# Kernel optimization log

Measured on AMD Instinct MI355X. Metric: run time of the kernel, lower is better.

The kernel has to match this reference:

```python
import jax, jax.numpy as jnp
import numpy as np

L, B, T, D, H, FF = 4, 8, 1024, 256, 8, 1024
DK = D // H
SCALE = 1.0 / np.sqrt(DK)


def _ln(x, g, b, eps=1e-6):
    m = jnp.mean(x, axis=-1, keepdims=True)
    v = jnp.mean(jnp.square(x - m), axis=-1, keepdims=True)
    return (x - m) * jax.lax.rsqrt(v + eps) * g + b


def _l2norm(x, eps=1e-8):
    n = jnp.sqrt(jnp.sum(jnp.square(x), axis=-1, keepdims=True))
    return x / jnp.maximum(n, eps)


def setup_inputs() -> dict:
    key = jax.random.key(0)
    ks = jax.random.split(key, 8)
    s = 0.02
    inp = {
        'x': jax.random.normal(ks[0], (B, T, D), dtype=jnp.float32),
        'padding_mask': jnp.zeros((B, T), dtype=bool),
        'ln1_g': jnp.ones((L, D), jnp.float32), 'ln1_b': jnp.zeros((L, D), jnp.float32),
        'qn_g': jnp.ones((L, D), jnp.float32), 'qn_b': jnp.zeros((L, D), jnp.float32),
        'Wqkv': jax.random.normal(ks[1], (L, 3 * D, D), jnp.float32) * s,
        'bqkv': jnp.zeros((L, 3 * D), jnp.float32),
        'Wo': jax.random.normal(ks[2], (L, D, D), jnp.float32) * s,
        'bo': jnp.zeros((L, D), jnp.float32),
        'ln2_g': jnp.ones((L, D), jnp.float32), 'ln2_b': jnp.zeros((L, D), jnp.float32),
        'W1': jax.random.normal(ks[3], (L, FF, D), jnp.float32) * s,
        'b1': jnp.zeros((L, FF), jnp.float32),
        'W2': jax.random.normal(ks[4], (L, D, FF), jnp.float32) * s,
        'b2': jnp.zeros((L, D), jnp.float32),
        'alpha': jnp.full((L,), 0.1, jnp.float32),
        'beta': jnp.full((L,), 0.1, jnp.float32),
    }
    return inp


def _block(x, pad_mask, p):
    (g1, bb1, qg, qb, wqkv, bqkv, wo, bo, g2, bb2, w1, b1, w2, b2, a, be) = p
    Bn, Tn, Dn = x.shape
    # --- SemiCausalAttention on norm1(x) ---
    xn = _ln(x, g1, bb1)
    h = _ln(xn, qg, qb)                      # q_norm LayerNorm
    qkv = h @ wqkv.T + bqkv                  # [B,T,3D]
    qkv = qkv.reshape(Bn, Tn, 3, H, DK).transpose(2, 0, 3, 1, 4)  # [3,B,H,T,dk]
    Q, K, V = qkv[0], qkv[1], qkv[2]
    Q = _l2norm(Q)
    K = _l2norm(K)
    scores = jnp.einsum('bhtd,bhsd->bhts', Q, K) * SCALE
    scores = jnp.clip(scores, -10.0, 10.0)
    causal = jnp.triu(jnp.ones((Tn, Tn), dtype=bool), k=1)        # True = future
    scores = jnp.where(causal[None, None], -10000.0, scores)
    scores = jnp.where(pad_mask[:, None, None, :], -10000.0, scores)
    attn = jax.nn.softmax(scores, axis=-1)
    ao = jnp.einsum('bhts,bhsd->bhtd', attn, V)                   # [B,H,T,dk]
    ao = ao.transpose(0, 2, 1, 3).reshape(Bn, Tn, Dn)
    attn_out = (ao @ wo.T + bo) * 0.5
    x = x + jnp.tanh(a) * attn_out
    # --- FFN ---
    f = _ln(x, g2, bb2)
    f = jax.nn.gelu(f @ w1.T + b1, approximate=False)
    f = f @ w2.T + b2
    x = x + jnp.tanh(be) * f
    return jnp.clip(x, -100.0, 100.0)


def reference(x, padding_mask, ln1_g, ln1_b, qn_g, qn_b, Wqkv, bqkv, Wo, bo,
              ln2_g, ln2_b, W1, b1, W2, b2, alpha, beta):
    params = (ln1_g, ln1_b, qn_g, qn_b, Wqkv, bqkv, Wo, bo,
              ln2_g, ln2_b, W1, b1, W2, b2, alpha, beta)

    def step(carry, p):
        return _block(carry, padding_mask, p), None

    out, _ = jax.lax.scan(step, x, params)
    return out
```

## Files before the change

kernel.cpp:

```cpp
#include <hip/hip_runtime.h>
#include <hip/hip_bf16.h>
#include <math.h>

#define BB 8
#define TT 1024
#define DD 256
#define HH 8
#define BT 8192

typedef __attribute__((ext_vector_type(4))) float f32x4;
typedef __attribute__((ext_vector_type(16))) float f32x16;
typedef __attribute__((ext_vector_type(8))) short short8;
typedef __attribute__((ext_vector_type(4))) short short4v;
typedef __attribute__((ext_vector_type(8))) __bf16 bf16x8;

__device__ inline float bf2f(short s) {
  unsigned int u = ((unsigned int)(unsigned short)s) << 16;
  return __builtin_bit_cast(float, u);
}
__device__ inline short f2bf(float f) {
  unsigned int u = __builtin_bit_cast(unsigned int, f);
  unsigned int lsb = (u >> 16) & 1u;
  u += 0x7fffu + lsb;
  return (short)(u >> 16);
}
__device__ inline unsigned int cvtpk(float lo, float hi) {
  unsigned int r;
  asm("v_cvt_pk_bf16_f32 %0, %1, %2" : "=v"(r) : "v"(lo), "v"(hi));
  return r;
}

__device__ inline f32x4 mfma16(short8 a, short8 b, f32x4 c) {
  return __builtin_amdgcn_mfma_f32_16x16x32_bf16(
      __builtin_bit_cast(bf16x8, a), __builtin_bit_cast(bf16x8, b), c, 0, 0, 0);
}
__device__ inline f32x16 mfma32(short8 a, short8 b, f32x16 c) {
  return __builtin_amdgcn_mfma_f32_32x32x16_bf16(
      __builtin_bit_cast(bf16x8, a), __builtin_bit_cast(bf16x8, b), c, 0, 0, 0);
}

__device__ inline void gload_lds16(void* lds, const void* g) {
  __builtin_amdgcn_global_load_lds(
      (const __attribute__((address_space(1))) unsigned int*)g,
      (__attribute__((address_space(3))) unsigned int*)lds, 16, 0, 0);
}

__global__ __launch_bounds__(256) void cvt_all(
    const float4* __restrict__ s0, short4v* __restrict__ d0, int n0,
    const float4* __restrict__ s1, short4v* __restrict__ d1, int n1,
    const float4* __restrict__ s2, short4v* __restrict__ d2, int n2,
    const float4* __restrict__ s3, short4v* __restrict__ d3, int n3)
{
  int i = blockIdx.x * 256 + threadIdx.x;
  const float4* s; short4v* d;
  if (i < n0) { s = s0 + i; d = d0 + i; }
  else if ((i -= n0) < n1) { s = s1 + i; d = d1 + i; }
  else if ((i -= n1) < n2) { s = s2 + i; d = d2 + i; }
  else if ((i -= n2) < n3) { s = s3 + i; d = d3 + i; }
  else return;
  float4 v = *s;
  short4v o;
  o[0] = f2bf(v.x); o[1] = f2bf(v.y); o[2] = f2bf(v.z); o[3] = f2bf(v.w);
  *d = o;
}

__global__ __launch_bounds__(256) void ln_kernel(
    const float* __restrict__ Xin,
    const float* __restrict__ g1, const float* __restrict__ b1,
    const float* __restrict__ g2, const float* __restrict__ b2,
    short* __restrict__ out)
{
  const int row = blockIdx.x * 4 + (threadIdx.x >> 6);
  const int lane = threadIdx.x & 63;
  const float4 v = *(const float4*)(Xin + (size_t)row * 256 + lane * 4);
  float y[4] = {v.x, v.y, v.z, v.w};

  float s = y[0] + y[1] + y[2] + y[3];
  #pragma unroll
  for (int m = 32; m >= 1; m >>= 1) s += __shfl_xor(s, m, 64);
  float mean = s * (1.0f / 256.0f);
  float sq = 0.f;
  #pragma unroll
  for (int i = 0; i < 4; ++i) { y[i] -= mean; sq += y[i] * y[i]; }
  #pragma unroll
  for (int m = 32; m >= 1; m >>= 1) sq += __shfl_xor(sq, m, 64);
  float rs = rsqrtf(sq * (1.0f / 256.0f) + 1e-6f);
  #pragma unroll
  for (int i = 0; i < 4; ++i) y[i] = y[i] * rs * g1[lane * 4 + i] + b1[lane * 4 + i];

  float s2 = y[0] + y[1] + y[2] + y[3];
  #pragma unroll
  for (int m = 32; m >= 1; m >>= 1) s2 += __shfl_xor(s2, m, 64);
  float m2 = s2 * (1.0f / 256.0f);
  float sq2 = 0.f;
  #pragma unroll
  for (int i = 0; i < 4; ++i) { y[i] -= m2; sq2 += y[i] * y[i]; }
  #pragma unroll
  for (int m = 32; m >= 1; m >>= 1) sq2 += __shfl_xor(sq2, m, 64);
  float rs2 = rsqrtf(sq2 * (1.0f / 256.0f) + 1e-6f);
  #pragma unroll
  for (int i = 0; i < 4; ++i) y[i] = y[i] * rs2 * g2[lane * 4 + i] + b2[lane * 4 + i];

  #pragma unroll
  for (int i = 0; i < 4; ++i) out[(size_t)row * 256 + lane * 4 + i] = f2bf(y[i]);
}

__global__ __launch_bounds__(256) void vtr_kernel(
    const short* __restrict__ qkv, short* __restrict__ vT)
{
  __shared__ short T_s[32][264];
  const int tid = threadIdx.x;
  const int bh = blockIdx.x >> 2;
  const int tc = blockIdx.x & 3;
  const int b = bh >> 3, h = bh & 7;
  const int t = tc * 256 + tid;
  const short* src = qkv + ((size_t)b * TT + t) * 768 + 512 + h * 32;
  short8 v0 = *(const short8*)(src);
  short8 v1 = *(const short8*)(src + 8);
  short8 v2 = *(const short8*)(src + 16);
  short8 v3 = *(const short8*)(src + 24);
  #pragma unroll
  for (int d = 0; d < 8; ++d) {
    T_s[d][tid] = v0[d];
    T_s[d + 8][tid] = v1[d];
    T_s[d + 16][tid] = v2[d];
    T_s[d + 24][tid] = v3[d];
  }
  __syncthreads();
  const int d = tid >> 3, toff = (tid & 7) * 32;
  short* dst = vT + ((size_t)bh * 32 + d) * 1024 + tc * 256 + toff;
  #pragma unroll
  for (int s = 0; s < 4; ++s)
    *(short8*)(dst + s * 8) = *(const short8*)&T_s[d][toff + s * 8];
}

template<int BN, int EPI>
__global__ __launch_bounds__(256) void gemm_bt(
    const short* __restrict__ A, const short* __restrict__ Bw,
    const float* __restrict__ bias, float* __restrict__ X,
    short* __restrict__ Obf, const float* __restrict__ scale_p,
    int M, int N, int K)
{
  constexpr int MI = (BN == 128) ? 4 : 2;
  __shared__ __align__(16) short A_s[128 * 128];
  __shared__ __align__(16) short B_s[BN * 128];
  const int tid = threadIdx.x;
  const int lane = tid & 63;
  const int w = tid >> 6;
  const int lo4 = lane & 15, hi2 = lane >> 4;
  int wm, wn0;
  if (BN == 128) { wm = (w >> 1) * 64; wn0 = (w & 1) * 64; }
  else           { wm = w * 32;        wn0 = 0; }
  const int bid = blockIdx.x + blockIdx.y * gridDim.x;
  const int nwg = gridDim.x * gridDim.y;
  const int wg = (bid & 7) * (nwg >> 3) + (bid >> 3);
  const int tM = (wg / gridDim.x) * 128, tN = (wg % gridDim.x) * BN;

  f32x4 acc[MI][4];
  #pragma unroll
  for (int i = 0; i < MI; ++i)
    #pragma unroll
    for (int j = 0; j < 4; ++j) acc[i][j] = (f32x4){0.f, 0.f, 0.f, 0.f};

  const int rswzA = ((wm + lo4) & 7) << 3;
  for (int k0 = 0; k0 < K; k0 += 128) {
    #pragma unroll
    for (int ri = 0; ri < 8; ++ri) {
      int o = ri * 2048 + tid * 8;
      int row = o >> 7;
      int col = (o & 127) ^ ((row & 7) << 3);
      gload_lds16(&A_s[ri * 2048 + w * 512], A + (size_t)(tM + row) * K + k0 + col);
    }
    #pragma unroll
    for (int ri = 0; ri < BN / 16; ++ri) {
      int o = ri * 2048 + tid * 8;
      int row = o >> 7;
      int col = (o & 127) ^ ((row & 7) << 3);
      gload_lds16(&B_s[ri * 2048 + w * 512], Bw + (size_t)(tN + row) * K + k0 + col);
    }
    __syncthreads();
    #pragma unroll
    for (int kc = 0; kc < 4; ++kc) {
      short8 af[MI], bfr[4];
      #pragma unroll
      for (int i = 0; i < MI; ++i) {
        int row = wm + i * 16 + lo4;
        af[i] = *(const short8*)&A_s[row * 128 + ((kc * 32 + hi2 * 8) ^ ((row & 7) << 3))];
      }
      #pragma unroll
      for (int j = 0; j < 4; ++j) {
        int row = wn0 + j * 16 + lo4;
        bfr[j] = *(const short8*)&B_s[row * 128 + ((kc * 32 + hi2 * 8) ^ ((row & 7) << 3))];
      }
      #pragma unroll
      for (int i = 0; i < MI; ++i)
        #pragma unroll
        for (int j = 0; j < 4; ++j)
          acc[i][j] = mfma16(af[i], bfr[j], acc[i][j]);
    }
    __syncthreads();
  }
  (void)rswzA;

  if (EPI == 4) {
    #pragma unroll
    for (int i = 0; i < MI; ++i)
      #pragma unroll
      for (int j = 0; j < 4; ++j)
        #pragma unroll
        for (int r = 0; r < 4; ++r)
          acc[i][j][r] += bias[tN + wn0 + j * 16 + lo4];
    if (tN < 512) {
      const float C2 = 0.25503489702966368f;
      const float sc = (tN < 256) ? C2 : 1.0f;
      #pragma unroll
      for (int i = 0; i < MI; ++i) {
        #pragma unroll
        for (int r = 0; r < 4; ++r) {
          float s01 = acc[i][0][r] * acc[i][0][r] + acc[i][1][r] * acc[i][1][r];
          float s23 = acc[i][2][r] * acc[i][2][r] + acc[i][3][r] * acc[i][3][r];
          #pragma unroll
          for (int m = 1; m <= 8; m <<= 1) {
            s01 += __shfl_xor(s01, m, 64);
            s23 += __shfl_xor(s23, m, 64);
          }
          float n01 = sc / fmaxf(sqrtf(s01), 1e-8f);
          float n23 = sc / fmaxf(sqrtf(s23), 1e-8f);
          acc[i][0][r] *= n01; acc[i][1][r] *= n01;
          acc[i][2][r] *= n23; acc[i][3][r] *= n23;
        }
      }
    }
    #pragma unroll
    for (int i = 0; i < MI; ++i)
      #pragma unroll
      for (int j = 0; j < 4; ++j)
        #pragma unroll
        for (int r = 0; r < 4; ++r) {
          int row = tM + wm + i * 16 + hi2 * 4 + r;
          int col = tN + wn0 + j * 16 + lo4;
          Obf[(size_t)row * N + col] = f2bf(acc[i][j][r]);
        }
    return;
  }

  #pragma unroll
  for (int i = 0; i < MI; ++i) {
    #pragma unroll
    for (int j = 0; j < 4; ++j) {
      #pragma unroll
      for (int r = 0; r < 4; ++r) {
        int row = tM + wm + i * 16 + hi2 * 4 + r;
        int col = tN + wn0 + j * 16 + lo4;
        float v = acc[i][j][r] + bias[col];
        size_t idx = (size_t)row * N + col;
        if (EPI == 2) {
          float gl = 0.5f * v * (1.0f + erff(v * 0.70710678118f));
          Obf[idx] = f2bf(gl);
        } else {
          Obf[idx] = f2bf(v);
        }
      }
    }
  }
}

template<int MODE>
__global__ __launch_bounds__(256) void gemm_ln(
    const short* __restrict__ A, const short* __restrict__ Bw,
    const float* __restrict__ bias, float* __restrict__ X,
    short* __restrict__ Obf, const float* __restrict__ scale_p,
    const float* __restrict__ gA, const float* __restrict__ bA,
    const float* __restrict__ gB, const float* __restrict__ bB,
    int K, int doLN)
{
  __shared__ __align__(16) short A_s[32 * 128];
  __shared__ __align__(16) short B_s[256 * 128];
  __shared__ float Red[2][32][4][2];
  const int tid = threadIdx.x;
  const int lane = tid & 63;
  const int w = tid >> 6;
  const int lo4 = lane & 15, hi2 = lane >> 4;
  const int tM = blockIdx.x * 32;

  f32x4 acc[2][4];
  #pragma unroll
  for (int i = 0; i < 2; ++i)
    #pragma unroll
    for (int j = 0; j < 4; ++j) acc[i][j] = (f32x4){0.f, 0.f, 0.f, 0.f};

  for (int k0 = 0; k0 < K; k0 += 128) {
    #pragma unroll
    for (int ri = 0; ri < 2; ++ri) {
      int o = ri * 2048 + tid * 8;
      int row = o >> 7;
      int col = (o & 127) ^ ((row & 7) << 3);
      gload_lds16(&A_s[ri * 2048 + w * 512], A + (size_t)(tM + row) * K + k0 + col);
    }
    #pragma unroll
    for (int ri = 0; ri < 16; ++ri) {
      int o = ri * 2048 + tid * 8;
      int row = o >> 7;
      int col = (o & 127) ^ ((row & 7) << 3);
      gload_lds16(&B_s[ri * 2048 + w * 512], Bw + (size_t)row * K + k0 + col);
    }
    __syncthreads();
    #pragma unroll
    for (int kc = 0; kc < 4; ++kc) {
      short8 af[2], bfr[4];
      #pragma unroll
      for (int i = 0; i < 2; ++i) {
        int row = i * 16 + lo4;
        af[i] = *(const short8*)&A_s[row * 128 + ((kc * 32 + hi2 * 8) ^ ((row & 7) << 3))];
      }
      #pragma unroll
      for (int j = 0; j < 4; ++j) {
        int row = w * 64 + j * 16 + lo4;
        bfr[j] = *(const short8*)&B_s[row * 128 + ((kc * 32 + hi2 * 8) ^ ((row & 7) << 3))];
      }
      #pragma unroll
      for (int i = 0; i < 2; ++i)
        #pragma unroll
        for (int j = 0; j < 4; ++j)
          acc[i][j] = mfma16(af[i], bfr[j], acc[i][j]);
    }
    __syncthreads();
  }

  const float ts = tanhf(scale_p[0]);
  float xv[2][4][4];
  #pragma unroll
  for (int i = 0; i < 2; ++i)
    #pragma unroll
    for (int j = 0; j < 4; ++j)
      #pragma unroll
      for (int r = 0; r < 4; ++r) {
        int row = i * 16 + hi2 * 4 + r;
        int col = w * 64 + j * 16 + lo4;
        float v = acc[i][j][r] + bias[col];
        size_t idx = (size_t)(tM + row) * 256 + col;
        float xn;
        if (MODE == 0) {
          xn = X[idx] + ts * 0.5f * v;
        } else {
          xn = X[idx] + ts * v;
          xn = fminf(100.f, fmaxf(-100.f, xn));
        }
        X[idx] = xn;
        xv[i][j][r] = xn;
      }

  if (!doLN) return;

  #pragma unroll
  for (int i = 0; i < 2; ++i)
    #pragma unroll
    for (int r = 0; r < 4; ++r) {
      float s = xv[i][0][r] + xv[i][1][r] + xv[i][2][r] + xv[i][3][r];
      float q = xv[i][0][r] * xv[i][0][r] + xv[i][1][r] * xv[i][1][r]
              + xv[i][2][r] * xv[i][2][r] + xv[i][3][r] * xv[i][3][r];
      #pragma unroll
      for (int m = 1; m <= 8; m <<= 1) { s += __shfl_xor(s, m, 64); q += __shfl_xor(q, m, 64); }
      if (lo4 == 0) { Red[0][i * 16 + hi2 * 4 + r][w][0] = s; Red[0][i * 16 + hi2 * 4 + r][w][1] = q; }
    }
  __syncthreads();
  #pragma unroll
  for (int i = 0; i < 2; ++i)
    #pragma unroll
    for (int r = 0; r < 4; ++r) {
      int row = i * 16 + hi2 * 4 + r;
      float s = Red[0][row][0][0] + Red[0][row][1][0] + Red[0][row][2][0] + Red[0][row][3][0];
      float q = Red[0][row][0][1] + Red[0][row][1][1] + Red[0][row][2][1] + Red[0][row][3][1];
      float mu = s * (1.0f / 256.0f);
      float var = q * (1.0f / 256.0f) - mu * mu;
      float rs = rsqrtf(var + 1e-6f);
      #pragma unroll
      for (int j = 0; j < 4; ++j) {
        int col = w * 64 + j * 16 + lo4;
        xv[i][j][r] = (xv[i][j][r] - mu) * rs * gA[col] + bA[col];
      }
    }

  if (MODE == 1) {
    #pragma unroll
    for (int i = 0; i < 2; ++i)
      #pragma unroll
      for (int r = 0; r < 4; ++r) {
        float s = xv[i][0][r] + xv[i][1][r] + xv[i][2][r] + xv[i][3][r];
        float q = xv[i][0][r] * xv[i][0][r] + xv[i][1][r] * xv[i][1][r]
                + xv[i][2][r] * xv[i][2][r] + xv[i][3][r] * xv[i][3][r];
        #pragma unroll
        for (int m = 1; m <= 8; m <<= 1) { s += __shfl_xor(s, m, 64); q += __shfl_xor(q, m, 64); }
        if (lo4 == 0) { Red[1][i * 16 + hi2 * 4 + r][w][0] = s; Red[1][i * 16 + hi2 * 4 + r][w][1] = q; }
      }
    __syncthreads();
    #pragma unroll
    for (int i = 0; i < 2; ++i)
      #pragma unroll
      for (int r = 0; r < 4; ++r) {
        int row = i * 16 + hi2 * 4 + r;
        float s = Red[1][row][0][0] + Red[1][row][1][0] + Red[1][row][2][0] + Red[1][row][3][0];
        float q = Red[1][row][0][1] + Red[1][row][1][1] + Red[1][row][2][1] + Red[1][row][3][1];
        float mu = s * (1.0f / 256.0f);
        float var = q * (1.0f / 256.0f) - mu * mu;
        float rs = rsqrtf(var + 1e-6f);
        #pragma unroll
        for (int j = 0; j < 4; ++j) {
          int col = w * 64 + j * 16 + lo4;
          xv[i][j][r] = (xv[i][j][r] - mu) * rs * gB[col] + bB[col];
        }
      }
  }

  #pragma unroll
  for (int i = 0; i < 2; ++i)
    #pragma unroll
    for (int j = 0; j < 4; ++j)
      #pragma unroll
      for (int r = 0; r < 4; ++r) {
        int row = i * 16 + hi2 * 4 + r;
        int col = w * 64 + j * 16 + lo4;
        Obf[(size_t)(tM + row) * 256 + col] = f2bf(xv[i][j][r]);
      }
}

__device__ __forceinline__ void pv_acc(const unsigned int* PKO, int half_,
                                       short8 vb, int hi1, f32x16& acc) {
  unsigned int keep0 = hi1 ? PKO[4 * half_ + 2] : PKO[4 * half_ + 0];
  unsigned int keep1 = hi1 ? PKO[4 * half_ + 3] : PKO[4 * half_ + 1];
  unsigned int send0 = hi1 ? PKO[4 * half_ + 0] : PKO[4 * half_ + 2];
  unsigned int send1 = hi1 ? PKO[4 * half_ + 1] : PKO[4 * half_ + 3];
  unsigned int r0 = (unsigned int)__shfl_xor((int)send0, 32, 64);
  unsigned int r1 = (unsigned int)__shfl_xor((int)send1, 32, 64);
  union { unsigned int u[4]; short8 s; } fa;
  fa.u[0] = hi1 ? r0 : keep0;
  fa.u[1] = hi1 ? r1 : keep1;
  fa.u[2] = hi1 ? keep0 : r0;
  fa.u[3] = hi1 ? keep1 : r1;
  acc = mfma32(fa.s, vb, acc);
}

template<bool KG1, bool M0, bool M1>
__device__ __forceinline__ void attn_tile(
    int t, const short* __restrict__ Kbase, const short* __restrict__ VTl,
    const short8* qb, unsigned int pm0, unsigned int pm1, int lo5, int hi1,
    f32x16& oaccA, f32x16& oaccB, float& rsum)
{
  const short* kp0 = Kbase + (size_t)(t * 64 + lo5) * 768;
  short8 k00 = *(const short8*)(kp0 + hi1 * 8);
  short8 k01 = *(const short8*)(kp0 + 16 + hi1 * 8);
  short8 k10, k11;
  if (KG1) {
    const short* kp1 = Kbase + (size_t)(t * 64 + 32 + lo5) * 768;
    k10 = *(const short8*)(kp1 + hi1 * 8);
    k11 = *(const short8*)(kp1 + 16 + hi1 * 8);
  }
  const short* vp = VTl + t * 64 + hi1 * 8;
  short8 vb0 = *(const short8*)(vp);
  short8 vb1 = *(const short8*)(vp + 16);
  short8 vb2, vb3;
  if (KG1) {
    vb2 = *(const short8*)(vp + 32);
    vb3 = *(const short8*)(vp + 48);
  }
  unsigned int pk0[8], pk1[8];
  {
    f32x16 z = (f32x16)0.0f;
    z = mfma32(k00, qb[0], z);
    z = mfma32(k01, qb[1], z);
    float pr[16];
    #pragma unroll
    for (int r = 0; r < 16; ++r) {
      float sv = __builtin_amdgcn_fmed3f(z[r], -14.4269504f, 14.4269504f);
      float pe;
      asm("v_exp_f32 %0, %1" : "=v"(pe) : "v"(sv));
      const int keyrel = (r & 3) + 8 * (r >> 2) + 4 * hi1;
      if (M0) pe = (keyrel > lo5) ? 0.f : pe;
      if (pm0) pe = ((pm0 >> keyrel) & 1u) ? 0.f : pe;
      pr[r] = pe;
      rsum += pe;
    }
    #pragma unroll
    for (int i = 0; i < 8; ++i) pk0[i] = cvtpk(pr[2 * i], pr[2 * i + 1]);
  }
  if (KG1) {
    f32x16 z = (f32x16)0.0f;
    z = mfma32(k10, qb[0], z);
    z = mfma32(k11, qb[1], z);
    float pr[16];
    #pragma unroll
    for (int r = 0; r < 16; ++r) {
      float sv = __builtin_amdgcn_fmed3f(z[r], -14.4269504f, 14.4269504f);
      float pe;
      asm("v_exp_f32 %0, %1" : "=v"(pe) : "v"(sv));
      const int keyrel = (r & 3) + 8 * (r >> 2) + 4 * hi1;
      if (M1) pe = (keyrel > lo5) ? 0.f : pe;
      if (pm1) pe = ((pm1 >> keyrel) & 1u) ? 0.f : pe;
      pr[r] = pe;
      rsum += pe;
    }
    #pragma unroll
    for (int i = 0; i < 8; ++i) pk1[i] = cvtpk(pr[2 * i], pr[2 * i + 1]);
  }
  pv_acc(pk0, 0, vb0, hi1, oaccA);
  pv_acc(pk0, 1, vb1, hi1, oaccB);
  if (KG1) {
    pv_acc(pk1, 0, vb2, hi1, oaccA);
    pv_acc(pk1, 1, vb3, hi1, oaccB);
  }
}

__global__ __launch_bounds__(256, 2) void attn_kernel(
    const short* __restrict__ qkv, const short* __restrict__ vT,
    const unsigned char* __restrict__ pad, short* __restrict__ ao)
{
  __shared__ float Red[2][17][64];
  const int tid = threadIdx.x, lane = tid & 63, w = tid >> 6;
  const int lo5 = lane & 31, hi1 = lane >> 5;
  const int bid = blockIdx.x;
  const int b = bid & 7;
  const int h = (bid >> 3) & 7;
  const int bj = bid >> 6;
  const int p = w >> 1;
  const int half = w & 1;
  const int j = p ? (31 - bj) : bj;
  const size_t rowbase = (size_t)b * TT;
  const int qrow = j * 32 + lo5;
  const int ntile = (j >> 1) + 1;

  const short* Kbase = qkv + rowbase * 768 + 256 + h * 32;
  const short* VTl = vT + ((size_t)(b * 8 + h) * 32 + lo5) * 1024;

  const ulonglong2 pv = *(const ulonglong2*)(pad + rowbase + lane * 16);
  const unsigned long long anyp = __ballot((pv.x | pv.y) != 0ull);

  short8 qb[2];
  #pragma unroll
  for (int c2 = 0; c2 < 2; ++c2)
    qb[c2] = *(const short8*)(qkv + (rowbase + qrow) * 768 + h * 32 + c2 * 16 + hi1 * 8);

  f32x16 oaccA = (f32x16)0.0f;
  f32x16 oaccB = (f32x16)0.0f;
  float rsum = 0.f;

  for (int t = half; t < ntile; t += 2) {
    unsigned long long pm = 0;
    if ((anyp >> (4 * t)) & 0xFull)
      pm = __ballot(pad[rowbase + t * 64 + lane] != 0);
    unsigned int pm0 = (unsigned int)pm, pm1 = (unsigned int)(pm >> 32);
    if (t + 1 < ntile)
      attn_tile<true, false, false>(t, Kbase, VTl, qb, pm0, pm1, lo5, hi1, oaccA, oaccB, rsum);
    else if (j & 1)
      attn_tile<true, false, true>(t, Kbase, VTl, qb, pm0, pm1, lo5, hi1, oaccA, oaccB, rsum);
    else
      attn_tile<false, true, false>(t, Kbase, VTl, qb, pm0, pm1, lo5, hi1, oaccA, oaccB, rsum);
  }

  if (half) {
    #pragma unroll
    for (int r = 0; r < 16; ++r) Red[p][r][lane] = oaccA[r] + oaccB[r];
    Red[p][16][lane] = rsum;
  }
  __syncthreads();
  if (!half) {
    #pragma unroll
    for (int r = 0; r < 16; ++r) oaccA[r] += oaccB[r] + Red[p][r][lane];
    rsum += Red[p][16][lane];
    rsum += __shfl_xor(rsum, 32, 64);
    float rinv = 1.0f / fmaxf(rsum, 1e-30f);
    #pragma unroll
    for (int r = 0; r < 16; ++r) {
      int ql = (r & 3) + 8 * (r >> 2) + 4 * hi1;
      float riv = __shfl(rinv, ql, 64);
      int qg = j * 32 + ql;
      ao[(rowbase + qg) * 256 + h * 32 + lo5] = f2bf(oaccA[r] * riv);
    }
  }
}

extern "C" void kernel_launch(void* const* d_in, const int* in_sizes, int n_in,
                              void* d_out, int out_size, void* d_ws, size_t ws_size,
                              hipStream_t stream) {
  const float* x_in  = (const float*)d_in[0];
  const unsigned char* pad = (const unsigned char*)d_in[1];
  const float* ln1_g = (const float*)d_in[2];
  const float* ln1_b = (const float*)d_in[3];
  const float* qn_g  = (const float*)d_in[4];
  const float* qn_b  = (const float*)d_in[5];
  const float* Wqkv  = (const float*)d_in[6];
  const float* bqkv  = (const float*)d_in[7];
  const float* Wo    = (const float*)d_in[8];
  const float* bo    = (const float*)d_in[9];
  const float* ln2_g = (const float*)d_in[10];
  const float* ln2_b = (const float*)d_in[11];
  const float* W1    = (const float*)d_in[12];
  const float* b1    = (const float*)d_in[13];
  const float* W2    = (const float*)d_in[14];
  const float* b2    = (const float*)d_in[15];
  const float* alpha = (const float*)d_in[16];
  const float* beta  = (const float*)d_in[17];

  char* ws = (char*)d_ws;
  size_t off = 0;
  short* wqkv_bf = (short*)(ws + off); off += (size_t)4 * 768 * 256 * 2;
  short* wo_bf   = (short*)(ws + off); off += (size_t)4 * 256 * 256 * 2;
  short* w1_bf   = (short*)(ws + off); off += (size_t)4 * 1024 * 256 * 2;
  short* w2_bf   = (short*)(ws + off); off += (size_t)4 * 256 * 1024 * 2;
  short* h_bf    = (short*)(ws + off); off += (size_t)BT * 256 * 2;
  short* qkv_bf  = (short*)(ws + off); off += (size_t)BT * 768 * 2;
  short* ao_bf   = (short*)(ws + off); off += (size_t)BT * 256 * 2;
  short* g_bf    = (short*)(ws + off); off += (size_t)BT * 1024 * 2;
  short* vT_bf   = (short*)(ws + off); off += (size_t)BT * 256 * 2;

  float* X = (float*)d_out;

  hipMemcpyAsync(d_out, x_in, (size_t)BT * DD * 4, hipMemcpyDeviceToDevice, stream);
  cvt_all<<<3072, 256, 0, stream>>>(
      (const float4*)Wqkv, (short4v*)wqkv_bf, 4 * 768 * 256 / 4,
      (const float4*)Wo,   (short4v*)wo_bf,   4 * 256 * 256 / 4,
      (const float4*)W1,   (short4v*)w1_bf,   4 * 1024 * 256 / 4,
      (const float4*)W2,   (short4v*)w2_bf,   4 * 256 * 1024 / 4);

  ln_kernel<<<2048, 256, 0, stream>>>(X, ln1_g, ln1_b, qn_g, qn_b, h_bf);

  for (int l = 0; l < 4; ++l) {
    gemm_bt<128, 4><<<dim3(6, 64), 256, 0, stream>>>(h_bf, wqkv_bf + (size_t)l * 768 * 256,
                                                     bqkv + l * 768, nullptr, qkv_bf, nullptr,
                                                     8192, 768, 256);
    vtr_kernel<<<256, 256, 0, stream>>>(qkv_bf, vT_bf);
    attn_kernel<<<1024, 256, 0, stream>>>(qkv_bf, vT_bf, pad, ao_bf);
    gemm_ln<0><<<256, 256, 0, stream>>>(ao_bf, wo_bf + (size_t)l * 256 * 256,
                                        bo + l * 256, X, h_bf, alpha + l,
                                        ln2_g + l * 256, ln2_b + l * 256,
                                        nullptr, nullptr, 256, 1);
    gemm_bt<128, 2><<<dim3(8, 64), 256, 0, stream>>>(h_bf, w1_bf + (size_t)l * 1024 * 256,
                                                     b1 + l * 1024, nullptr, g_bf, nullptr,
                                                     8192, 1024, 256);
    const int nl = (l < 3) ? (l + 1) : 0;
    gemm_ln<1><<<256, 256, 0, stream>>>(g_bf, w2_bf + (size_t)l * 256 * 1024,
                                        b2 + l * 256, X, h_bf, beta + l,
                                        ln1_g + nl * 256, ln1_b + nl * 256,
                                        qn_g + nl * 256, qn_b + nl * 256,
                                        1024, (l < 3) ? 1 : 0);
  }
}
```

Before: 380.7 us.

## Write Q/K/V head-major from QKV GEMM and double-buffer GEMM K-tiles

The QKV GEMM epilogue now scatters Q, K and V into separate head-major [B*H, T, 32] buffers, so attention and the V transpose read contiguous 64-byte rows instead of 768-element strided rows. Separately, both GEMM kernels switch from a single 128-wide K tile to double-buffered 64-wide K tiles, issuing the next tile's loads before computing the current one to overlap memory with MFMA. LDS footprint stays the same. The epilogue stores become more scattered, and the loop has twice as many barriers.

```diff
diff --git a/kernel.cpp b/kernel.cpp
--- a/kernel.cpp
+++ b/kernel.cpp
@@ -106,15 +106,14 @@
 }
 
 __global__ __launch_bounds__(256) void vtr_kernel(
-    const short* __restrict__ qkv, short* __restrict__ vT)
+    const short* __restrict__ Vc, short* __restrict__ vT)
 {
   __shared__ short T_s[32][264];
   const int tid = threadIdx.x;
   const int bh = blockIdx.x >> 2;
   const int tc = blockIdx.x & 3;
-  const int b = bh >> 3, h = bh & 7;
   const int t = tc * 256 + tid;
-  const short* src = qkv + ((size_t)b * TT + t) * 768 + 512 + h * 32;
+  const short* src = Vc + ((size_t)(bh << 10) + t) * 32;
   short8 v0 = *(const short8*)(src);
   short8 v1 = *(const short8*)(src + 8);
   short8 v2 = *(const short8*)(src + 16);
@@ -137,13 +136,13 @@
 template<int BN, int EPI>
 __global__ __launch_bounds__(256) void gemm_bt(
     const short* __restrict__ A, const short* __restrict__ Bw,
-    const float* __restrict__ bias, float* __restrict__ X,
-    short* __restrict__ Obf, const float* __restrict__ scale_p,
+    const float* __restrict__ bias,
+    short* __restrict__ O0, short* __restrict__ O1, short* __restrict__ O2,
     int M, int N, int K)
 {
   constexpr int MI = (BN == 128) ? 4 : 2;
-  __shared__ __align__(16) short A_s[128 * 128];
-  __shared__ __align__(16) short B_s[BN * 128];
+  __shared__ __align__(16) short A_s[2][128 * 64];
+  __shared__ __align__(16) short B_s[2][BN * 64];
   const int tid = threadIdx.x;
   const int lane = tid & 63;
   const int w = tid >> 6;
@@ -162,35 +161,41 @@
     #pragma unroll
     for (int j = 0; j < 4; ++j) acc[i][j] = (f32x4){0.f, 0.f, 0.f, 0.f};
 
-  const int rswzA = ((wm + lo4) & 7) << 3;
-  for (int k0 = 0; k0 < K; k0 += 128) {
-    #pragma unroll
-    for (int ri = 0; ri < 8; ++ri) {
+  auto stage = [&](int buf, int k0) {
+    #pragma unroll
+    for (int ri = 0; ri < 4; ++ri) {
       int o = ri * 2048 + tid * 8;
-      int row = o >> 7;
-      int col = (o & 127) ^ ((row & 7) << 3);
-      gload_lds16(&A_s[ri * 2048 + w * 512], A + (size_t)(tM + row) * K + k0 + col);
-    }
-    #pragma unroll
-    for (int ri = 0; ri < BN / 16; ++ri) {
+      int row = o >> 6;
+      int col = (o & 63) ^ ((row & 7) << 3);
+      gload_lds16(&A_s[buf][ri * 2048 + w * 512], A + (size_t)(tM + row) * K + k0 + col);
+    }
+    #pragma unroll
+    for (int ri = 0; ri < BN / 32; ++ri) {
       int o = ri * 2048 + tid * 8;
-      int row = o >> 7;
-      int col = (o & 127) ^ ((row & 7) << 3);
-      gload_lds16(&B_s[ri * 2048 + w * 512], Bw + (size_t)(tN + row) * K + k0 + col);
-    }
-    __syncthreads();
-    #pragma unroll
-    for (int kc = 0; kc < 4; ++kc) {
+      int row = o >> 6;
+      int col = (o & 63) ^ ((row & 7) << 3);
+      gload_lds16(&B_s[buf][ri * 2048 + w * 512], Bw + (size_t)(tN + row) * K + k0 + col);
+    }
+  };
+
+  const int nt = K >> 6;
+  stage(0, 0);
+  __syncthreads();
+  for (int t = 0; t < nt; ++t) {
+    const int cur = t & 1;
+    if (t + 1 < nt) stage(cur ^ 1, (t + 1) << 6);
+    #pragma unroll
+    for (int kc = 0; kc < 2; ++kc) {
       short8 af[MI], bfr[4];
       #pragma unroll
       for (int i = 0; i < MI; ++i) {
         int row = wm + i * 16 + lo4;
-        af[i] = *(const short8*)&A_s[row * 128 + ((kc * 32 + hi2 * 8) ^ ((row & 7) << 3))];
+        af[i] = *(const short8*)&A_s[cur][row * 64 + ((kc * 32 + hi2 * 8) ^ ((row & 7) << 3))];
       }
       #pragma unroll
       for (int j = 0; j < 4; ++j) {
         int row = wn0 + j * 16 + lo4;
-        bfr[j] = *(const short8*)&B_s[row * 128 + ((kc * 32 + hi2 * 8) ^ ((row & 7) << 3))];
+        bfr[j] = *(const short8*)&B_s[cur][row * 64 + ((kc * 32 + hi2 * 8) ^ ((row & 7) << 3))];
       }
       #pragma unroll
       for (int i = 0; i < MI; ++i)
@@ -200,7 +205,6 @@
     }
     __syncthreads();
   }
-  (void)rswzA;
 
   if (EPI == 4) {
     #pragma unroll
@@ -231,6 +235,7 @@
         }
       }
     }
+    short* dst = (tN < 256) ? O0 : (tN < 512) ? O1 : O2;
     #pragma unroll
     for (int i = 0; i < MI; ++i)
       #pragma unroll
@@ -238,8 +243,10 @@
         #pragma unroll
         for (int r = 0; r < 4; ++r) {
           int row = tM + wm + i * 16 + hi2 * 4 + r;
-          int col = tN + wn0 + j * 16 + lo4;
-          Obf[(size_t)row * N + col] = f2bf(acc[i][j][r]);
+          int colr = (tN + wn0 + j * 16 + lo4) & 255;
+          int h = colr >> 5, d = colr & 31;
+          size_t idx = (((size_t)((row >> 10) * 8 + h) << 10) | (size_t)(row & 1023)) * 32 + d;
+          dst[idx] = f2bf(acc[i][j][r]);
         }
     return;
   }
@@ -256,9 +263,9 @@
         size_t idx = (size_t)row * N + col;
         if (EPI == 2) {
           float gl = 0.5f * v * (1.0f + erff(v * 0.70710678118f));
-          Obf[idx] = f2bf(gl);
+          O0[idx] = f2bf(gl);
         } else {
-          Obf[idx] = f2bf(v);
+          O0[idx] = f2bf(v);
         }
       }
     }
@@ -274,8 +281,8 @@
     const float* __restrict__ gB, const float* __restrict__ bB,
     int K, int doLN)
 {
-  __shared__ __align__(16) short A_s[32 * 128];
-  __shared__ __align__(16) short B_s[256 * 128];
+  __shared__ __align__(16) short A_s[2][32 * 64];
+  __shared__ __align__(16) short B_s[2][256 * 64];
   __shared__ float Red[2][32][4][2];
   const int tid = threadIdx.x;
   const int lane = tid & 63;
@@ -289,34 +296,40 @@
     #pragma unroll
     for (int j = 0; j < 4; ++j) acc[i][j] = (f32x4){0.f, 0.f, 0.f, 0.f};
 
-  for (int k0 = 0; k0 < K; k0 += 128) {
-    #pragma unroll
-    for (int ri = 0; ri < 2; ++ri) {
+  auto stage = [&](int buf, int k0) {
+    {
+      int o = tid * 8;
+      int row = o >> 6;
+      int col = (o & 63) ^ ((row & 7) << 3);
+      gload_lds16(&A_s[buf][w * 512], A + (size_t)(tM + row) * K + k0 + col);
+    }
+    #pragma unroll
+    for (int ri = 0; ri < 8; ++ri) {
       int o = ri * 2048 + tid * 8;
-      int row = o >> 7;
-      int col = (o & 127) ^ ((row & 7) << 3);
-      gload_lds16(&A_s[ri * 2048 + w * 512], A + (size_t)(tM + row) * K + k0 + col);
-    }
-    #pragma unroll
-    for (int ri = 0; ri < 16; ++ri) {
-      int o = ri * 2048 + tid * 8;
-      int row = o >> 7;
-      int col = (o & 127) ^ ((row & 7) << 3);
-      gload_lds16(&B_s[ri * 2048 + w * 512], Bw + (size_t)row * K + k0 + col);
-    }
-    __syncthreads();
-    #pragma unroll
-    for (int kc = 0; kc < 4; ++kc) {
+      int row = o >> 6;
+      int col = (o & 63) ^ ((row & 7) << 3);
+      gload_lds16(&B_s[buf][ri * 2048 + w * 512], Bw + (size_t)row * K + k0 + col);
+    }
+  };
+
+  const int nt = K >> 6;
+  stage(0, 0);
+  __syncthreads();
+  for (int t = 0; t < nt; ++t) {
+    const int cur = t & 1;
+    if (t + 1 < nt) stage(cur ^ 1, (t + 1) << 6);
+    #pragma unroll
+    for (int kc = 0; kc < 2; ++kc) {
       short8 af[2], bfr[4];
       #pragma unroll
       for (int i = 0; i < 2; ++i) {
         int row = i * 16 + lo4;
-        af[i] = *(const short8*)&A_s[row * 128 + ((kc * 32 + hi2 * 8) ^ ((row & 7) << 3))];
+        af[i] = *(const short8*)&A_s[cur][row * 64 + ((kc * 32 + hi2 * 8) ^ ((row & 7) << 3))];
       }
       #pragma unroll
       for (int j = 0; j < 4; ++j) {
         int row = w * 64 + j * 16 + lo4;
-        bfr[j] = *(const short8*)&B_s[row * 128 + ((kc * 32 + hi2 * 8) ^ ((row & 7) << 3))];
+        bfr[j] = *(const short8*)&B_s[cur][row * 64 + ((kc * 32 + hi2 * 8) ^ ((row & 7) << 3))];
       }
       #pragma unroll
       for (int i = 0; i < 2; ++i)
@@ -446,12 +459,12 @@
     const short8* qb, unsigned int pm0, unsigned int pm1, int lo5, int hi1,
     f32x16& oaccA, f32x16& oaccB, float& rsum)
 {
-  const short* kp0 = Kbase + (size_t)(t * 64 + lo5) * 768;
+  const short* kp0 = Kbase + (size_t)(t * 64 + lo5) * 32;
   short8 k00 = *(const short8*)(kp0 + hi1 * 8);
   short8 k01 = *(const short8*)(kp0 + 16 + hi1 * 8);
   short8 k10, k11;
   if (KG1) {
-    const short* kp1 = Kbase + (size_t)(t * 64 + 32 + lo5) * 768;
+    const short* kp1 = Kbase + (size_t)(t * 64 + 32 + lo5) * 32;
     k10 = *(const short8*)(kp1 + hi1 * 8);
     k11 = *(const short8*)(kp1 + 16 + hi1 * 8);
   }
@@ -511,8 +524,9 @@
 }
 
 __global__ __launch_bounds__(256, 2) void attn_kernel(
-    const short* __restrict__ qkv, const short* __restrict__ vT,
-    const unsigned char* __restrict__ pad, short* __restrict__ ao)
+    const short* __restrict__ Qp, const short* __restrict__ Kp,
+    const short* __restrict__ vT, const unsigned char* __restrict__ pad,
+    short* __restrict__ ao)
 {
   __shared__ float Red[2][17][64];
   const int tid = threadIdx.x, lane = tid & 63, w = tid >> 6;
@@ -525,11 +539,12 @@
   const int half = w & 1;
   const int j = p ? (31 - bj) : bj;
   const size_t rowbase = (size_t)b * TT;
+  const int bh = b * 8 + h;
   const int qrow = j * 32 + lo5;
   const int ntile = (j >> 1) + 1;
 
-  const short* Kbase = qkv + rowbase * 768 + 256 + h * 32;
-  const short* VTl = vT + ((size_t)(b * 8 + h) * 32 + lo5) * 1024;
+  const short* Kbase = Kp + ((size_t)bh << 10) * 32;
+  const short* VTl = vT + ((size_t)bh * 32 + lo5) * 1024;
 
   const ulonglong2 pv = *(const ulonglong2*)(pad + rowbase + lane * 16);
   const unsigned long long anyp = __ballot((pv.x | pv.y) != 0ull);
@@ -537,7 +552,7 @@
   short8 qb[2];
   #pragma unroll
   for (int c2 = 0; c2 < 2; ++c2)
-    qb[c2] = *(const short8*)(qkv + (rowbase + qrow) * 768 + h * 32 + c2 * 16 + hi1 * 8);
+    qb[c2] = *(const short8*)(Qp + (((size_t)bh << 10) + qrow) * 32 + c2 * 16 + hi1 * 8);
 
   f32x16 oaccA = (f32x16)0.0f;
   f32x16 oaccB = (f32x16)0.0f;
@@ -607,10 +622,12 @@
   short* w1_bf   = (short*)(ws + off); off += (size_t)4 * 1024 * 256 * 2;
   short* w2_bf   = (short*)(ws + off); off += (size_t)4 * 256 * 1024 * 2;
   short* h_bf    = (short*)(ws + off); off += (size_t)BT * 256 * 2;
-  short* qkv_bf  = (short*)(ws + off); off += (size_t)BT * 768 * 2;
+  short* Qp_bf   = (short*)(ws + off); off += (size_t)BT * 256 * 2;
+  short* Kp_bf   = (short*)(ws + off); off += (size_t)BT * 256 * 2;
+  short* Vc_bf   = (short*)(ws + off); off += (size_t)BT * 256 * 2;
+  short* vT_bf   = (short*)(ws + off); off += (size_t)BT * 256 * 2;
   short* ao_bf   = (short*)(ws + off); off += (size_t)BT * 256 * 2;
   short* g_bf    = (short*)(ws + off); off += (size_t)BT * 1024 * 2;
-  short* vT_bf   = (short*)(ws + off); off += (size_t)BT * 256 * 2;
 
   float* X = (float*)d_out;
 
@@ -625,16 +642,16 @@
 
   for (int l = 0; l < 4; ++l) {
     gemm_bt<128, 4><<<dim3(6, 64), 256, 0, stream>>>(h_bf, wqkv_bf + (size_t)l * 768 * 256,
-                                                     bqkv + l * 768, nullptr, qkv_bf, nullptr,
+                                                     bqkv + l * 768, Qp_bf, Kp_bf, Vc_bf,
                                                      8192, 768, 256);
-    vtr_kernel<<<256, 256, 0, stream>>>(qkv_bf, vT_bf);
-    attn_kernel<<<1024, 256, 0, stream>>>(qkv_bf, vT_bf, pad, ao_bf);
+    vtr_kernel<<<256, 256, 0, stream>>>(Vc_bf, vT_bf);
+    attn_kernel<<<1024, 256, 0, stream>>>(Qp_bf, Kp_bf, vT_bf, pad, ao_bf);
     gemm_ln<0><<<256, 256, 0, stream>>>(ao_bf, wo_bf + (size_t)l * 256 * 256,
                                         bo + l * 256, X, h_bf, alpha + l,
                                         ln2_g + l * 256, ln2_b + l * 256,
                                         nullptr, nullptr, 256, 1);
     gemm_bt<128, 2><<<dim3(8, 64), 256, 0, stream>>>(h_bf, w1_bf + (size_t)l * 1024 * 256,
-                                                     b1 + l * 1024, nullptr, g_bf, nullptr,
+                                                     b1 + l * 1024, g_bf, nullptr, nullptr,
                                                      8192, 1024, 256);
     const int nl = (l < 3) ? (l + 1) : 0;
     gemm_ln<1><<<256, 256, 0, stream>>>(g_bf, w2_bf + (size_t)l * 256 * 1024,
```

After: 366.3 us. -3.8%, faster.
